# Optimization experiments

Measured on AMD Instinct MI355X. Metric: run time of the kernel, lower is better.

## Reference

```python
import jax, jax.numpy as jnp
import numpy as np

# ---- static config (mirrors ProposalLayerModule param) ----
FEAT_STRIDE = 16
PRE_NMS_TOPN = 6000
POST_NMS_TOPN = 300
NMS_THRESH = 0.7
MIN_SIZE = 16.0
NUM_ANCHORS = 9


def _generate_anchors():
    """Replicates generate_anchors(base_size=16, ratios=[0.5,1,2], scales=[8,16,32])."""
    base = np.array([0.0, 0.0, 15.0, 15.0])
    ratios = np.array([0.5, 1.0, 2.0])
    scales = np.array([8.0, 16.0, 32.0])
    w = base[2] - base[0] + 1.0
    h = base[3] - base[1] + 1.0
    xc = base[0] + 0.5 * (w - 1.0)
    yc = base[1] + 0.5 * (h - 1.0)
    size = w * h
    ws = np.round(np.sqrt(size / ratios))
    hs = np.round(ws * ratios)
    ratio_anchors = np.stack([xc - 0.5 * (ws - 1), yc - 0.5 * (hs - 1),
                              xc + 0.5 * (ws - 1), yc + 0.5 * (hs - 1)], axis=1)
    out = []
    for a in ratio_anchors:
        aw = a[2] - a[0] + 1.0
        ah = a[3] - a[1] + 1.0
        axc = a[0] + 0.5 * (aw - 1.0)
        ayc = a[1] + 0.5 * (ah - 1.0)
        ws2 = aw * scales
        hs2 = ah * scales
        out.append(np.stack([axc - 0.5 * (ws2 - 1), ayc - 0.5 * (hs2 - 1),
                             axc + 0.5 * (ws2 - 1), ayc + 0.5 * (hs2 - 1)], axis=1))
    return np.concatenate(out, axis=0).astype(np.float32)  # (9, 4)

_ANCHORS = _generate_anchors()


def _nms_keep(iou, valid, thresh):
    """Greedy NMS over score-sorted boxes. Returns boolean keep mask."""
    n = iou.shape[0]
    idx = jnp.arange(n)
    def body(i, keep):
        sup = keep[i] & (iou[i] > thresh) & (idx > i)
        return keep & jnp.logical_not(sup)
    return jax.lax.fori_loop(0, n, body, valid)


def setup_inputs() -> dict:
    key = jax.random.key(0)
    k1, k2 = jax.random.split(key)
    H, W = 128, 192
    scores = jax.random.normal(k1, (1, 2 * NUM_ANCHORS, H, W), dtype=jnp.float32)
    # small deltas so exp(dw), exp(dh) stay in a realistic range
    bbox_deltas = jax.random.normal(k2, (1, 4 * NUM_ANCHORS, H, W), dtype=jnp.float32) * 0.1
    im_info = jnp.array([H * FEAT_STRIDE, W * FEAT_STRIDE, 1.0], dtype=jnp.float32)
    return {"scores": scores, "bbox_deltas": bbox_deltas, "im_info": im_info}


def reference(scores, bbox_deltas, im_info):
    A = NUM_ANCHORS
    s = scores[0, A:]                      # (A, H, W) fg scores
    Hf, Wf = s.shape[1], s.shape[2]
    # shifts, matching torch.meshgrid default indexing='ij' (x-major flatten)
    shift_x = jnp.arange(Wf, dtype=jnp.float32) * FEAT_STRIDE
    shift_y = jnp.arange(Hf, dtype=jnp.float32) * FEAT_STRIDE
    sx, sy = jnp.meshgrid(shift_x, shift_y, indexing='ij')   # (W, H)
    shifts = jnp.stack([sx.ravel(), sy.ravel(), sx.ravel(), sy.ravel()], axis=1)  # (K,4)
    anchors = (jnp.asarray(_ANCHORS)[None, :, :] + shifts[:, None, :]).reshape(-1, 4)  # (K*A,4)

    deltas = jnp.transpose(bbox_deltas[0], (1, 2, 0)).reshape(-1, 4)  # (H*W*A,4)
    sc = jnp.transpose(s, (1, 2, 0)).reshape(-1)                      # (H*W*A,)

    # bbox_transform_inv
    widths = anchors[:, 2] - anchors[:, 0] + 1.0
    heights = anchors[:, 3] - anchors[:, 1] + 1.0
    ctr_x = anchors[:, 0] + 0.5 * widths
    ctr_y = anchors[:, 1] + 0.5 * heights
    dx, dy, dw, dh = deltas[:, 0], deltas[:, 1], deltas[:, 2], deltas[:, 3]
    pcx = dx * widths + ctr_x
    pcy = dy * heights + ctr_y
    pw = jnp.exp(dw) * widths
    ph = jnp.exp(dh) * heights
    x1 = pcx - 0.5 * pw
    y1 = pcy - 0.5 * ph
    x2 = pcx + 0.5 * pw
    y2 = pcy + 0.5 * ph

    # clip_boxes
    x1 = jnp.clip(x1, 0.0, im_info[1] - 1.0)
    x2 = jnp.clip(x2, 0.0, im_info[1] - 1.0)
    y1 = jnp.clip(y1, 0.0, im_info[0] - 1.0)
    y2 = jnp.clip(y2, 0.0, im_info[0] - 1.0)
    boxes = jnp.stack([x1, y1, x2, y2], axis=1)

    # _filter_boxes (as a mask, jit-friendly)
    ms = MIN_SIZE * im_info[2]
    valid = ((x2 - x1 + 1.0) >= ms) & ((y2 - y1 + 1.0) >= ms)
    masked_sc = jnp.where(valid, sc, -jnp.inf)

    # sort by score descending + pre_nms_topN
    top_s, top_i = jax.lax.top_k(masked_sc, PRE_NMS_TOPN)
    b = boxes[top_i]                       # (PRE, 4), score-sorted
    vld = jnp.isfinite(top_s)

    # torchvision-style IoU (no +1) + greedy NMS
    area = (b[:, 2] - b[:, 0]) * (b[:, 3] - b[:, 1])
    ix1 = jnp.maximum(b[:, None, 0], b[None, :, 0])
    iy1 = jnp.maximum(b[:, None, 1], b[None, :, 1])
    ix2 = jnp.minimum(b[:, None, 2], b[None, :, 2])
    iy2 = jnp.minimum(b[:, None, 3], b[None, :, 3])
    inter = jnp.clip(ix2 - ix1, 0.0) * jnp.clip(iy2 - iy1, 0.0)
    iou = inter / jnp.maximum(area[:, None] + area[None, :] - inter, 1e-9)
    keep = _nms_keep(iou, vld, NMS_THRESH)

    # first post_nms_topN kept boxes (fixed-size, zero-padded), prepend batch idx 0
    cum = jnp.cumsum(keep.astype(jnp.int32))
    pos = jnp.where(keep & (cum <= POST_NMS_TOPN), cum - 1, POST_NMS_TOPN)
    rows = jnp.concatenate([jnp.zeros((PRE_NMS_TOPN, 1), jnp.float32), b], axis=1)
    out = jnp.zeros((POST_NMS_TOPN + 1, 5), jnp.float32).at[pos].set(rows)[:POST_NMS_TOPN]
    return out
```

## Files before the change

kernel.cpp:

```cpp
#include <hip/hip_runtime.h>

#define NCELL 24576
#define NTOT  221184
#define NBIN13 8192
#define TOPN  6000
#define POSTN 300
#define NPADR 6016
#define NW    94
#define CW    8
#define NCHUNK 12
#define NCB   16
#define SLOT  1024
#define CAP2  (NCB*SLOT)

__global__ void decode_kernel(const float* __restrict__ scores,
                              const float* __restrict__ deltas,
                              const float* __restrict__ iminfo,
                              float4* __restrict__ boxes,
                              unsigned* __restrict__ skeys,
                              unsigned short* __restrict__ skeys16) {
#pragma clang fp contract(off)
    int c = blockIdx.x * blockDim.x + threadIdx.x;
    if (c >= NCELL) return;
    const float AW[9] = {184.f,368.f,736.f,128.f,256.f,512.f, 88.f,176.f,352.f};
    const float AH[9] = { 96.f,192.f,384.f,128.f,256.f,512.f,176.f,352.f,704.f};
    float sx = (float)((c >> 7) << 4);
    float sy = (float)((c & 127) << 4);
    float imh = iminfo[0], imw = iminfo[1], ims = iminfo[2];
    float xhi = imw - 1.0f, yhi = imh - 1.0f;
    float ms = 16.0f * ims;
    float ctrx = sx + 8.0f, ctry = sy + 8.0f;
    const float* sbase = scores + 9 * NCELL + c;
    const float* dbase = deltas + c;
#pragma unroll
    for (int a = 0; a < 9; ++a) {
        float sc = sbase[a * NCELL];
        float dx = dbase[(4 * a + 0) * NCELL];
        float dy = dbase[(4 * a + 1) * NCELL];
        float dw = dbase[(4 * a + 2) * NCELL];
        float dh = dbase[(4 * a + 3) * NCELL];
        float pcx = dx * AW[a] + ctrx;
        float pcy = dy * AH[a] + ctry;
        float pw = expf(dw) * AW[a];
        float ph = expf(dh) * AH[a];
        float x1 = pcx - 0.5f * pw;
        float y1 = pcy - 0.5f * ph;
        float x2 = pcx + 0.5f * pw;
        float y2 = pcy + 0.5f * ph;
        x1 = fminf(fmaxf(x1, 0.0f), xhi);
        x2 = fminf(fmaxf(x2, 0.0f), xhi);
        y1 = fminf(fmaxf(y1, 0.0f), yhi);
        y2 = fminf(fmaxf(y2, 0.0f), yhi);
        bool valid = ((x2 - x1 + 1.0f) >= ms) && ((y2 - y1 + 1.0f) >= ms);
        unsigned u = __float_as_uint(sc);
        unsigned key = (u & 0x80000000u) ? ~u : (u | 0x80000000u);
        if (!valid) key = 0x007FFFFFu;
        boxes[a * NCELL + c] = make_float4(x1, y1, x2, y2);
        skeys[a * NCELL + c] = key;
        skeys16[a * NCELL + c] = (unsigned short)(key >> 16);
    }
}

__global__ __launch_bounds__(1024) void compactT_kernel(const unsigned* __restrict__ skeys,
                                                        const unsigned short* __restrict__ skeys16,
                                                        unsigned* __restrict__ meta16,
                                                        unsigned long long* __restrict__ cbuf) {
    __shared__ unsigned hist[NBIN13];
    __shared__ unsigned psum[1024];
    __shared__ unsigned csum[256];
    __shared__ unsigned sB, sAbove, sT, sCount;
    int tid = threadIdx.x, bid = blockIdx.x;
    for (int b = tid; b < NBIN13; b += 1024) hist[b] = 0u;
    if (tid == 0) sCount = 0u;
    __syncthreads();
    const uint4* s16 = (const uint4*)skeys16;
    for (int q = tid; q < NTOT / 8; q += 1024) {
        uint4 u = s16[q];
        atomicAdd(&hist[(u.x & 0xFFFFu) >> 3], 1u);
        atomicAdd(&hist[u.x >> 19], 1u);
        atomicAdd(&hist[(u.y & 0xFFFFu) >> 3], 1u);
        atomicAdd(&hist[u.y >> 19], 1u);
        atomicAdd(&hist[(u.z & 0xFFFFu) >> 3], 1u);
        atomicAdd(&hist[u.z >> 19], 1u);
        atomicAdd(&hist[(u.w & 0xFFFFu) >> 3], 1u);
        atomicAdd(&hist[u.w >> 19], 1u);
    }
    __syncthreads();
    unsigned s = 0;
#pragma unroll
    for (int q = 0; q < 8; ++q) s += hist[tid * 8 + q];
    psum[tid] = s;
    __syncthreads();
    if (tid < 256)
        csum[tid] = psum[tid * 4] + psum[tid * 4 + 1] + psum[tid * 4 + 2] + psum[tid * 4 + 3];
    __syncthreads();
    if (tid < 64) {
        int lane = tid;
        unsigned c0 = csum[lane * 4 + 0], c1 = csum[lane * 4 + 1];
        unsigned c2 = csum[lane * 4 + 2], c3 = csum[lane * 4 + 3];
        unsigned ls = c0 + c1 + c2 + c3;
        unsigned v = ls;
#pragma unroll
        for (int o = 1; o < 64; o <<= 1) {
            unsigned t = __shfl_down(v, o, 64);
            if (lane + o < 64) v += t;
        }
        unsigned sufExcl = v - ls;
        unsigned a3 = sufExcl;
        unsigned a2 = a3 + c3;
        unsigned a1 = a2 + c2;
        unsigned a0 = a1 + c1;
        if (a0 < TOPN && a0 + c0 >= TOPN) { sB = lane * 4 + 0; sAbove = a0; }
        if (a1 < TOPN && a1 + c1 >= TOPN) { sB = lane * 4 + 1; sAbove = a1; }
        if (a2 < TOPN && a2 + c2 >= TOPN) { sB = lane * 4 + 2; sAbove = a2; }
        if (a3 < TOPN && a3 + c3 >= TOPN) { sB = lane * 4 + 3; sAbove = a3; }
    }
    __syncthreads();
    if (tid < 32) {
        unsigned B = sB, above = sAbove;
        unsigned h = hist[B * 32 + tid];
        unsigned v = h;
#pragma unroll
        for (int o = 1; o < 32; o <<= 1) {
            unsigned t = __shfl_down(v, o, 64);
            if (tid + o < 32) v += t;
        }
        unsigned sufExcl = v - h;
        unsigned ab = above + sufExcl;
        if (ab < TOPN && ab + h >= TOPN) sT = B * 32 + tid;
    }
    __syncthreads();
    unsigned T = sT;
    int base = bid * (NTOT / NCB);
    const uint4* s4b = (const uint4*)(skeys + base);
    for (int q = tid; q < (NTOT / NCB) / 4; q += 1024) {
        uint4 u = s4b[q];
        unsigned k4[4] = {u.x, u.y, u.z, u.w};
#pragma unroll
        for (int k = 0; k < 4; ++k) {
            if ((k4[k] >> 19) >= T) {
                unsigned lp = atomicAdd(&sCount, 1u);
                if (lp < SLOT) {
                    int m = base + 4 * q + k;
                    unsigned n = (unsigned)((m % NCELL) * 9 + (m / NCELL));
                    cbuf[(bid << 10) + lp] =
                        ((unsigned long long)k4[k] << 32) | (unsigned long long)(~n);
                }
            }
        }
    }
    __syncthreads();
    unsigned cnt = sCount; if (cnt > SLOT) cnt = SLOT;
    for (int e = cnt + tid; e < SLOT; e += 1024) cbuf[(bid << 10) + e] = 0ULL;
    if (tid == 0) meta16[bid] = cnt;
}

__global__ __launch_bounds__(256) void rankscatter_kernel(const unsigned long long* __restrict__ cbuf,
                                                          const unsigned* __restrict__ meta16,
                                                          const float4* __restrict__ boxes,
                                                          float4* __restrict__ sortedbox) {
    __shared__ unsigned long long jk[512];
    __shared__ unsigned scnt[NCB];
    int tid = threadIdx.x;
    if (tid < NCB) scnt[tid] = meta16[tid];
    __syncthreads();
    int i = blockIdx.x * 32 + (tid >> 3);
    int slice = tid & 7;
    unsigned long long ki = cbuf[i];
    unsigned cr = 0;
    for (int jt = 0; jt < CAP2 / 512; ++jt) {
        int b = jt >> 1;
        unsigned cb = scnt[b];
        if ((jt & 1) ? (cb <= 512u) : (cb == 0u)) continue;
        __syncthreads();
        for (int q = tid; q < 512; q += 256) jk[q] = cbuf[(jt << 9) + q];
        __syncthreads();
#pragma unroll 8
        for (int j = 0; j < 64; ++j) cr += (jk[slice + (j << 3)] > ki) ? 1u : 0u;
    }
    cr += __shfl_down(cr, 4, 8);
    cr += __shfl_down(cr, 2, 8);
    cr += __shfl_down(cr, 1, 8);
    if (slice == 0 && ki != 0ULL && cr < NPADR) {
        unsigned n = ~(unsigned)ki;
        unsigned m = (n % 9u) * (unsigned)NCELL + (n / 9u);
        sortedbox[cr] = boxes[m];
    }
}

__global__ __launch_bounds__(256) void matrix_kernel(const float4* __restrict__ sortedbox,
                                                     unsigned long long* __restrict__ rowr,
                                                     unsigned long long* __restrict__ diagw,
                                                     unsigned long long* __restrict__ diagT) {
#pragma clang fp contract(off)
    __shared__ float4 jb[256];
    __shared__ float  ja[256];
    int tid = threadIdx.x;
    int lane = tid & 63, wave = tid >> 6;
    int i0 = blockIdx.y << 6;
    int i = i0 + lane;
    int w = (blockIdx.x << 2) + wave;
    int jbase = blockIdx.x << 8;
    unsigned long long word = 0ULL;

    if (jbase + 255 > i0) {
        int jg = jbase + tid;
        float4 v = (jg < NPADR) ? sortedbox[jg] : make_float4(0.f, 0.f, 0.f, 0.f);
        jb[tid] = v;
        ja[tid] = (v.z - v.x) * (v.w - v.y);
        __syncthreads();
        if (w < NW && ((w << 6) + 63) > i) {
            float4 bi = sortedbox[i];
            float ai = (bi.z - bi.x) * (bi.w - bi.y);
            int jl0 = wave << 6;
            int jg0 = (w << 6);
#pragma unroll 8
            for (int j = 0; j < 64; ++j) {
                float4 bj = jb[jl0 + j];
                float aj = ja[jl0 + j];
                float iw = fminf(bi.z, bj.z) - fmaxf(bi.x, bj.x);
                float ih = fminf(bi.w, bj.w) - fmaxf(bi.y, bj.y);
                iw = fmaxf(iw, 0.0f);
                ih = fmaxf(ih, 0.0f);
                float inter = iw * ih;
                float denom = fmaxf(ai + aj - inter, 1e-9f);
                bool sup = (jg0 + j > i) && (inter / denom > 0.7f);
                word |= (unsigned long long)sup << j;
            }
        }
    }
    if (w < NW) {
        if (w >= (i >> 6))
            rowr[(size_t)i * NW + w] = word;
        if ((i >> 9) == (w >> 3))
            diagw[((size_t)w << 9) + (i & 511)] = word;
        if (w == (i >> 6)) {
            unsigned long long col = 0ULL;
#pragma unroll
            for (int jbit = 0; jbit < 64; ++jbit) {
                unsigned long long m = __ballot((word >> jbit) & 1ULL);
                if (lane == jbit) col = m;
            }
            diagT[((size_t)w << 6) + lane] = col;
        }
    }
}

__global__ __launch_bounds__(512) void scan_kernel(const unsigned long long* __restrict__ rowr,
                                                   const unsigned long long* __restrict__ diagw,
                                                   const unsigned long long* __restrict__ diagT,
                                                   const float4* __restrict__ sortedbox,
                                                   float* __restrict__ out) {
    __shared__ __align__(16) unsigned long long cblk[2][CW * 512];
    __shared__ unsigned long long ldsT[2][CW * 64];
    __shared__ unsigned long long gm[128];
    __shared__ int keptArr[POSTN];
    __shared__ int s_kept, s_done;
    int tid = threadIdx.x;
    int lane = tid & 63, wave = tid >> 6;

    if (tid < 128) gm[tid] = (tid == 93) ? ~((1ULL << 48) - 1) : 0ULL;
    if (tid == 0) { s_kept = 0; s_done = 0; }
    for (int e = tid; e < CW * 512; e += 512) cblk[0][e] = diagw[e];
    for (int e = tid; e < CW * 64; e += 512) ldsT[0][e] = diagT[e];
    __syncthreads();

    int keptPrev = 0;
    int keptPrev2 = 0;
    for (int c = 0; c < NCHUNK; ++c) {
        int buf = c & 1, nbuf = buf ^ 1;
        int wbase = c * CW;
        if (wave == 0) {
            unsigned long long dgT[CW];
#pragma unroll
            for (int q = 0; q < CW; ++q) dgT[q] = ldsT[buf][(q << 6) + lane];
            unsigned long long lowmask = (1ULL << lane) - 1ULL;
            int kept = s_kept;
            int done = 0;
            for (int q = 0; q < CW && wbase + q < NW; ++q) {
                int w = wbase + q;
                unsigned long long live = ~gm[w];
                if (w == NW - 1) live &= (1ULL << 48) - 1;
                if (!live) continue;
                bool alive = (live >> lane) & 1ULL;
                unsigned long long x = live;
                for (;;) {
                    bool sup = (dgT[q] & x & lowmask) != 0ULL;
                    unsigned long long xn = __ballot(alive && !sup);
                    if (xn == x) break;
                    x = xn;
                }
                unsigned long long kb = x;
                if (kb) {
                    int nk = __popcll(kb);
                    int myr = __popcll(kb & lowmask);
                    if (((kb >> lane) & 1ULL) && (kept + myr < POSTN))
                        keptArr[kept + myr] = (w << 6) + lane;
                    kept += nk;
                    if (kept >= POSTN) { kept = POSTN; done = 1; }
                }
                if (kb && !done && q < CW - 1) {
                    bool act = (lane > q) && (lane < CW);
                    int base = (lane << 9) + (q << 6);
                    unsigned long long acc = 0ULL;
                    unsigned long long t = kb;
                    while (t) {
                        int b0 = __ffsll((unsigned long long)t) - 1; t &= t - 1;
                        int b1 = 0, b2 = 0, b3 = 0, nb = 1;
                        if (t) { b1 = __ffsll((unsigned long long)t) - 1; t &= t - 1; nb = 2; }
                        if (t) { b2 = __ffsll((unsigned long long)t) - 1; t &= t - 1; nb = 3; }
                        if (t) { b3 = __ffsll((unsigned long long)t) - 1; t &= t - 1; nb = 4; }
                        unsigned long long r0 = act ? cblk[buf][base + b0] : 0ULL;
                        unsigned long long r1 = (act && nb > 1) ? cblk[buf][base + b1] : 0ULL;
                        unsigned long long r2 = (act && nb > 2) ? cblk[buf][base + b2] : 0ULL;
                        unsigned long long r3 = (act && nb > 3) ? cblk[buf][base + b3] : 0ULL;
                        acc |= (r0 | r1) | (r2 | r3);
                    }
                    if (act && acc) atomicOr(&gm[wbase + lane], acc);
                }
                if (done) break;
            }
            if (lane == 0) { s_kept = kept; s_done = done; }
        } else if (wave < 4) {
            if (c + 1 < NCHUNK) {
                int t = tid - 64;
                int wb2 = wbase + CW;
                int rb2 = wb2 << 6;
                for (int e = t; e < CW * 512; e += 192) {
                    int q = e >> 9, r = e & 511;
                    cblk[nbuf][e] = (wb2 + q < NW && rb2 + r < NPADR)
                        ? diagw[((size_t)(wb2 + q) << 9) + r] : 0ULL;
                }
                for (int e = t; e < CW * 64; e += 192) {
                    int q = e >> 6;
                    ldsT[nbuf][e] = (wb2 + q < NW) ? diagT[((size_t)wb2 << 6) + e] : 0ULL;
                }
            }
        } else {
            int nw2 = NW - (wbase + CW);
            int nr2 = keptPrev - keptPrev2;
            if (c > 0 && nr2 > 0 && nw2 > 0) {
                int t = tid - 256;
                int tot = nr2 * nw2;
                for (int idx = t; idx < tot; idx += 256) {
                    int s = idx / nw2, wo = idx - s * nw2;
                    int row = keptArr[keptPrev2 + s];
                    unsigned long long v = rowr[(size_t)row * NW + (wbase + CW) + wo];
                    if (v) atomicOr(&gm[wbase + CW + wo], v);
                }
            }
        }
        __syncthreads();
        int keptNow = s_kept;
        bool fin = (s_done != 0) || (c == NCHUNK - 1);
        if (!fin && keptNow > keptPrev) {
            int w1 = wbase + CW;
            int nw1 = NW - w1; if (nw1 > CW) nw1 = CW;
            int wo = tid & 7;
            for (int s = keptPrev + (tid >> 3); s < keptNow; s += 64) {
                if (wo < nw1) {
                    int row = keptArr[s];
                    unsigned long long v = rowr[(size_t)row * NW + w1 + wo];
                    if (v) atomicOr(&gm[w1 + wo], v);
                }
            }
        }
        keptPrev2 = keptPrev;
        keptPrev = keptNow;
        if (fin) break;
        __syncthreads();
    }
    __syncthreads();

    int kept = s_kept;
    for (int k = tid; k < POSTN; k += 512) {
        float4 bb = make_float4(0.f, 0.f, 0.f, 0.f);
        if (k < kept) bb = sortedbox[keptArr[k]];
        out[k * 5 + 0] = 0.0f;
        out[k * 5 + 1] = bb.x;
        out[k * 5 + 2] = bb.y;
        out[k * 5 + 3] = bb.z;
        out[k * 5 + 4] = bb.w;
    }
}

extern "C" void kernel_launch(void* const* d_in, const int* in_sizes, int n_in,
                              void* d_out, int out_size, void* d_ws, size_t ws_size,
                              hipStream_t stream) {
    const float* scores = (const float*)d_in[0];
    const float* deltas = (const float*)d_in[1];
    const float* iminfo = (const float*)d_in[2];
    char* w = (char*)d_ws;
    float4*   boxes = (float4*)w;
    unsigned* skeys = (unsigned*)(w + 3538944);
    unsigned long long* rowr = (unsigned long long*)w;
    unsigned* meta16 = (unsigned*)(w + 4786176);
    unsigned long long* cbuf = (unsigned long long*)(w + 4786240);
    float4* sortedbox = (float4*)(w + 4917312);
    unsigned long long* diagw = (unsigned long long*)(w + 5013568);
    unsigned long long* diagT = (unsigned long long*)(w + 5398592);
    unsigned short* skeys16 = (unsigned short*)(w + 5446720);
    float* out = (float*)d_out;

    decode_kernel<<<NCELL / 256, 256, 0, stream>>>(scores, deltas, iminfo, boxes, skeys, skeys16);
    compactT_kernel<<<NCB, 1024, 0, stream>>>(skeys, skeys16, meta16, cbuf);
    rankscatter_kernel<<<CAP2 / 32, 256, 0, stream>>>(cbuf, meta16, boxes, sortedbox);
    matrix_kernel<<<dim3(24, 94), 256, 0, stream>>>(sortedbox, rowr, diagw, diagT);
    scan_kernel<<<1, 512, 0, stream>>>(rowr, diagw, diagT, sortedbox, out);
}
```

Measured before the change: 156.9 us.

## Prefetch next-chunk suppression rows into LDS and drop the per-chunk second barrier

The NMS scan kernel previously applied the rows kept in the just-finished chunk to the next chunk's masks with a global-memory pass between two barriers each iteration. Now the helper waves prefetch the 512 rows of the current chunk's next-chunk suppression words into a new double-buffered LDS array. Wave 0 then ORs the previous chunk's kept rows from LDS at the start of its step, and one barrier per chunk goes away. Within a chunk, the live masks stay in registers and spread via shuffles and 8-lane reductions instead of LDS atomics. This costs extra LDS (64 KB) and unconditional prefetch traffic, which may cut occupancy, though the kernel is a single block anyway.

```diff
diff --git a/kernel.cpp b/kernel.cpp
--- a/kernel.cpp
+++ b/kernel.cpp
@@ -252,6 +252,7 @@
                                                    const float4* __restrict__ sortedbox,
                                                    float* __restrict__ out) {
     __shared__ __align__(16) unsigned long long cblk[2][CW * 512];
+    __shared__ __align__(16) unsigned long long sdg[2][512 * 8];
     __shared__ unsigned long long ldsT[2][CW * 64];
     __shared__ unsigned long long gm[128];
     __shared__ int keptArr[POSTN];
@@ -265,22 +266,34 @@
     for (int e = tid; e < CW * 64; e += 512) ldsT[0][e] = diagT[e];
     __syncthreads();
 
-    int keptPrev = 0;
-    int keptPrev2 = 0;
+    int kA = 0;
+    int kB = 0;
     for (int c = 0; c < NCHUNK; ++c) {
         int buf = c & 1, nbuf = buf ^ 1;
         int wbase = c * CW;
         if (wave == 0) {
+            int grp = lane >> 3, sub = lane & 7;
+            int myw = wbase + grp;
+            unsigned long long g_own = (myw < NW) ? gm[myw] : ~0ULL;
+            {
+                unsigned long long acc = 0ULL;
+                for (int s = kA + sub; s < kB; s += 8)
+                    acc |= sdg[buf][((keptArr[s] & 511) << 3) + grp];
+                acc |= __shfl_xor(acc, 1, 64);
+                acc |= __shfl_xor(acc, 2, 64);
+                acc |= __shfl_xor(acc, 4, 64);
+                g_own |= acc;
+            }
             unsigned long long dgT[CW];
 #pragma unroll
             for (int q = 0; q < CW; ++q) dgT[q] = ldsT[buf][(q << 6) + lane];
             unsigned long long lowmask = (1ULL << lane) - 1ULL;
-            int kept = s_kept;
+            int kept = kB;
             int done = 0;
             for (int q = 0; q < CW && wbase + q < NW; ++q) {
-                int w = wbase + q;
-                unsigned long long live = ~gm[w];
-                if (w == NW - 1) live &= (1ULL << 48) - 1;
+                unsigned long long lv = __shfl(g_own, q << 3, 64);
+                unsigned long long live = ~lv;
+                if (wbase + q == NW - 1) live &= (1ULL << 48) - 1;
                 if (!live) continue;
                 bool alive = (live >> lane) & 1ULL;
                 unsigned long long x = live;
@@ -295,28 +308,23 @@
                     int nk = __popcll(kb);
                     int myr = __popcll(kb & lowmask);
                     if (((kb >> lane) & 1ULL) && (kept + myr < POSTN))
-                        keptArr[kept + myr] = (w << 6) + lane;
+                        keptArr[kept + myr] = ((wbase + q) << 6) + lane;
                     kept += nk;
                     if (kept >= POSTN) { kept = POSTN; done = 1; }
                 }
                 if (kb && !done && q < CW - 1) {
-                    bool act = (lane > q) && (lane < CW);
-                    int base = (lane << 9) + (q << 6);
                     unsigned long long acc = 0ULL;
-                    unsigned long long t = kb;
-                    while (t) {
-                        int b0 = __ffsll((unsigned long long)t) - 1; t &= t - 1;
-                        int b1 = 0, b2 = 0, b3 = 0, nb = 1;
-                        if (t) { b1 = __ffsll((unsigned long long)t) - 1; t &= t - 1; nb = 2; }
-                        if (t) { b2 = __ffsll((unsigned long long)t) - 1; t &= t - 1; nb = 3; }
-                        if (t) { b3 = __ffsll((unsigned long long)t) - 1; t &= t - 1; nb = 4; }
-                        unsigned long long r0 = act ? cblk[buf][base + b0] : 0ULL;
-                        unsigned long long r1 = (act && nb > 1) ? cblk[buf][base + b1] : 0ULL;
-                        unsigned long long r2 = (act && nb > 2) ? cblk[buf][base + b2] : 0ULL;
-                        unsigned long long r3 = (act && nb > 3) ? cblk[buf][base + b3] : 0ULL;
-                        acc |= (r0 | r1) | (r2 | r3);
+                    if (grp > q) {
+                        int base = (grp << 9) + (q << 6) + sub;
+#pragma unroll
+                        for (int k = 0; k < 8; ++k)
+                            if ((kb >> (sub + (k << 3))) & 1ULL)
+                                acc |= cblk[buf][base + (k << 3)];
                     }
-                    if (act && acc) atomicOr(&gm[wbase + lane], acc);
+                    acc |= __shfl_xor(acc, 1, 64);
+                    acc |= __shfl_xor(acc, 2, 64);
+                    acc |= __shfl_xor(acc, 4, 64);
+                    if (grp > q) g_own |= acc;
                 }
                 if (done) break;
             }
@@ -335,40 +343,31 @@
                     int q = e >> 6;
                     ldsT[nbuf][e] = (wb2 + q < NW) ? diagT[((size_t)wb2 << 6) + e] : 0ULL;
                 }
+                int rowbase = c << 9;
+                for (int e = t; e < 512 * 8; e += 192) {
+                    int r = e >> 3, q = e & 7;
+                    sdg[nbuf][e] = (wb2 + q < NW)
+                        ? rowr[(size_t)(rowbase + r) * NW + wb2 + q] : 0ULL;
+                }
             }
         } else {
             int nw2 = NW - (wbase + CW);
-            int nr2 = keptPrev - keptPrev2;
+            int nr2 = kB - kA;
             if (c > 0 && nr2 > 0 && nw2 > 0) {
                 int t = tid - 256;
                 int tot = nr2 * nw2;
                 for (int idx = t; idx < tot; idx += 256) {
                     int s = idx / nw2, wo = idx - s * nw2;
-                    int row = keptArr[keptPrev2 + s];
+                    int row = keptArr[kA + s];
                     unsigned long long v = rowr[(size_t)row * NW + (wbase + CW) + wo];
                     if (v) atomicOr(&gm[wbase + CW + wo], v);
                 }
             }
         }
         __syncthreads();
-        int keptNow = s_kept;
-        bool fin = (s_done != 0) || (c == NCHUNK - 1);
-        if (!fin && keptNow > keptPrev) {
-            int w1 = wbase + CW;
-            int nw1 = NW - w1; if (nw1 > CW) nw1 = CW;
-            int wo = tid & 7;
-            for (int s = keptPrev + (tid >> 3); s < keptNow; s += 64) {
-                if (wo < nw1) {
-                    int row = keptArr[s];
-                    unsigned long long v = rowr[(size_t)row * NW + w1 + wo];
-                    if (v) atomicOr(&gm[w1 + wo], v);
-                }
-            }
-        }
-        keptPrev2 = keptPrev;
-        keptPrev = keptNow;
-        if (fin) break;
-        __syncthreads();
+        kA = kB;
+        kB = s_kept;
+        if (s_done != 0 || c == NCHUNK - 1) break;
     }
     __syncthreads();
 
```

After: 161.1 us. +2.6%, slower.
